# Kernel tuning notes

Hardware: AMD Instinct MI355X
Metric: run time of the kernel (lower is better)

The kernel has to match this reference:

```python
import jax, jax.numpy as jnp
import numpy as np

H = 128          # rnn_hid_size
SEQ_LEN = 2048
B = 4096
IN = 2           # SELECT_SIZE * 2


def _uniform(key, shape, stdv):
    return jax.random.uniform(key, shape, jnp.float32, -stdv, stdv)


def setup_inputs() -> dict:
    key = jax.random.key(0)
    ks = jax.random.split(key, 20)
    values = jax.random.normal(ks[0], (B, SEQ_LEN, 3), jnp.float32)
    masks = (jax.random.uniform(ks[1], (B, SEQ_LEN)) > 0.5).astype(jnp.float32)
    deltas = jax.random.uniform(ks[2], (B, SEQ_LEN, 3), jnp.float32)
    eval_masks = (jax.random.uniform(ks[3], (B, SEQ_LEN)) > 0.5).astype(jnp.float32)
    s = 1.0 / np.sqrt(H)
    params = {
        'Wih0': _uniform(ks[4], (4 * H, IN), s), 'Whh0': _uniform(ks[5], (4 * H, H), s),
        'bih0': _uniform(ks[6], (4 * H,), s), 'bhh0': _uniform(ks[7], (4 * H,), s),
        'Wih1': _uniform(ks[8], (4 * H, IN), s), 'Whh1': _uniform(ks[9], (4 * H, H), s),
        'bih1': _uniform(ks[10], (4 * H,), s), 'bhh1': _uniform(ks[11], (4 * H,), s),
        'td_W': _uniform(ks[12], (H, 1), s), 'td_b': _uniform(ks[13], (H,), s),
        'hr_W': _uniform(ks[14], (1, H), 1.0 / np.sqrt(H)), 'hr_b': _uniform(ks[15], (1,), 1.0 / np.sqrt(H)),
    }
    return dict(values=values, masks=masks, deltas=deltas, eval_masks=eval_masks, **params)


def _lstm_cell(x, h, c, Wih, Whh, bih, bhh):
    g = x @ Wih.T + bih + h @ Whh.T + bhh            # [B, 4H]
    i, f, gg, o = jnp.split(g, 4, axis=1)
    c2 = jax.nn.sigmoid(f) * c + jax.nn.sigmoid(i) * jnp.tanh(gg)
    h2 = jax.nn.sigmoid(o) * jnp.tanh(c2)
    return h2, c2


def reference(values, masks, deltas, eval_masks,
              Wih0, Whh0, bih0, bhh0, Wih1, Whh1, bih1, bhh1,
              td_W, td_b, hr_W, hr_b):
    bsize = values.shape[0]
    # time-major sequences for scan
    x_seq = jnp.transpose(values[:, :, 2:3], (1, 0, 2))      # [T, B, 1]
    m_seq = jnp.transpose(masks[:, :, None], (1, 0, 2))      # [T, B, 1]
    d_seq = jnp.transpose(deltas[:, :, 2:3], (1, 0, 2))      # [T, B, 1]
    in1_seq = jnp.transpose(values[:, :, 0:2], (1, 0, 2))    # [T, B, 2]

    h0 = jnp.zeros((bsize, H), jnp.float32)
    h1 = jnp.zeros((bsize, H), jnp.float32)
    c1 = jnp.zeros((bsize, H), jnp.float32)
    loss0 = jnp.zeros((), jnp.float32)

    def step(carry, inp):
        h0, h1, c1, loss = carry
        x_y, m_y, d_y, in1 = inp
        gamma_h = jnp.exp(-jax.nn.relu(d_y @ td_W.T + td_b))  # [B, H]
        x_h = h0 @ hr_W.T + hr_b                              # [B, 1]
        x_c = m_y * x_y + (1.0 - m_y) * x_h
        loss = loss + jnp.sum(jnp.square(x_y - x_h) * m_y) / (jnp.sum(m_y) + 1e-05)
        h1n, c1n = _lstm_cell(in1, h1, c1, Wih1, Whh1, bih1, bhh1)
        h1n = h1n * gamma_h
        inputs = jnp.concatenate([x_c, m_y], axis=1)          # [B, 2]
        h0n, _ = _lstm_cell(inputs, h1n, c1n, Wih0, Whh0, bih0, bhh0)
        return (h0n, h1n, c1n, loss), x_c

    (_, _, _, loss), imp = jax.lax.scan(step, (h0, h1, c1, loss0),
                                        (x_seq, m_seq, d_seq, in1_seq))
    imputations = jnp.transpose(imp, (1, 0, 2))               # [B, T, 1]
    evals = values[:, :, 2:3]
    return (loss, imputations, eval_masks[:, :, None], evals, masks[:, :, None])
```

## Files before the change

### kernel.cpp

```cpp
#include <hip/hip_runtime.h>

typedef __attribute__((ext_vector_type(8))) short bf16x8;
typedef __attribute__((ext_vector_type(4))) float f32x4;

#define L2E 1.4426950408889634f

__device__ __forceinline__ short f2bf(float x){
  unsigned u = __builtin_bit_cast(unsigned, x);
  u += 0x7fffu + ((u >> 16) & 1u);
  return (short)(u >> 16);
}
__device__ __forceinline__ float sigm(float x){
  float e = __builtin_amdgcn_exp2f(-x * L2E);
  return __builtin_amdgcn_rcpf(1.0f + e);
}
__device__ __forceinline__ float tanh_(float x){
  float e = __builtin_amdgcn_exp2f(x * (2.0f * L2E));
  return 1.0f - 2.0f * __builtin_amdgcn_rcpf(1.0f + e);
}

__global__ __launch_bounds__(512, 2)
void rios_main(const float* __restrict__ values, const float* __restrict__ masks,
               const float* __restrict__ deltas,
               const float* __restrict__ Wih0, const float* __restrict__ Whh0,
               const float* __restrict__ bih0, const float* __restrict__ bhh0,
               const float* __restrict__ Wih1, const float* __restrict__ Whh1,
               const float* __restrict__ bih1, const float* __restrict__ bhh1,
               const float* __restrict__ td_W, const float* __restrict__ td_b,
               const float* __restrict__ hr_W, const float* __restrict__ hr_b,
               float* __restrict__ out, float* __restrict__ lossws)
{
  __shared__ short hb[2][16][136];
  __shared__ float xh_part[8][16];
  __shared__ float xc_s[16];
  __shared__ float sA[2][5][16][16];

  const int tid = threadIdx.x;
  const int w  = tid >> 6;
  const int l  = tid & 63;
  const int q  = l >> 4;
  const int c  = l & 15;
  const int q4 = q << 2;
  const int u  = (w << 4) + c;
  const long long bb = (long long)blockIdx.x * 16;

  bf16x8 wf[2][4][4];
  {
    const float* WhhA[2] = { Whh1, Whh0 };
    #pragma unroll
    for (int cell = 0; cell < 2; ++cell)
      #pragma unroll
      for (int gi = 0; gi < 4; ++gi)
        #pragma unroll
        for (int kt = 0; kt < 4; ++kt){
          const float* rp = WhhA[cell] + (((gi << 7) + u) << 7) + (kt << 5) + (q << 3);
          bf16x8 f;
          #pragma unroll
          for (int j = 0; j < 8; ++j) f[j] = f2bf(rp[j]);
          wf[cell][gi][kt] = f;
        }
  }
  float wi[2][4][2], bs[2][4];
  {
    const float* WihA[2] = { Wih1, Wih0 };
    const float* bihA[2] = { bih1, bih0 };
    const float* bhhA[2] = { bhh1, bhh0 };
    #pragma unroll
    for (int cell = 0; cell < 2; ++cell)
      #pragma unroll
      for (int gi = 0; gi < 4; ++gi){
        int rg = (gi << 7) + u;
        wi[cell][gi][0] = WihA[cell][rg * 2];
        wi[cell][gi][1] = WihA[cell][rg * 2 + 1];
        bs[cell][gi]    = bihA[cell][rg] + bhhA[cell][rg];
      }
  }
  const float tdw = td_W[u], tdbv = td_b[u], hrw = hr_W[u], hrb = hr_b[0];

  {
    short* hz = &hb[0][0][0];
    for (int i = tid; i < 16 * 136; i += 512) hz[i] = 0;
    if (tid < 128) ((float*)xh_part)[tid] = 0.f;
  }

  const int isV = (tid < 192);
  const int isD = (tid >= 192 && tid < 384);
  const int isM = (tid >= 384 && tid < 448);
  int lb = 0, lp = 0;
  if (isV){ lb = tid / 12;        lp = tid % 12; }
  else if (isD){ lb = (tid-192)/12; lp = (tid-192)%12; }
  else if (isM){ lb = (tid-384)/4;  lp = (tid-384)%4; }
  const float* ldbase = nullptr;
  if (isV)      ldbase = values + ((bb + lb) * 2048LL) * 3 + lp * 4;
  else if (isD) ldbase = deltas + ((bb + lb) * 2048LL) * 3 + lp * 4;
  else if (isM) ldbase = masks  +  (bb + lb) * 2048LL      + lp * 4;

  auto write_stage = [&](int buf, f32x4 r){
    if (isV){
      #pragma unroll
      for (int j = 0; j < 4; ++j){ int idx = lp * 4 + j; sA[buf][idx % 3][idx / 3][lb] = r[j]; }
    } else if (isD){
      #pragma unroll
      for (int j = 0; j < 4; ++j){ int idx = lp * 4 + j; if (idx % 3 == 2) sA[buf][4][idx / 3][lb] = r[j]; }
    } else if (isM){
      #pragma unroll
      for (int j = 0; j < 4; ++j){ sA[buf][3][lp * 4 + j][lb] = r[j]; }
    }
  };

  if (tid < 448){
    f32x4 st = *(const f32x4*)(ldbase);
    write_stage(0, st);
  }
  __syncthreads();

  f32x4 c1 = {0.f, 0.f, 0.f, 0.f};

  for (int cc = 0; cc < 128; ++cc){
    const int cb = cc & 1;
    f32x4 nst;
    if (cc + 1 < 128 && tid < 448){
      long long t0 = (long long)(cc + 1) * 16;
      nst = *(const f32x4*)(ldbase + (isM ? t0 : t0 * 3));
    }
    #pragma unroll 2
    for (int tt = 0; tt < 16; ++tt){
      const int t = (cc << 4) + tt;
      const int p = tt & 1;

      f32x4 v0v = *(const f32x4*)&sA[cb][0][tt][q4];
      f32x4 v1v = *(const f32x4*)&sA[cb][1][tt][q4];
      f32x4 dv  = *(const f32x4*)&sA[cb][4][tt][q4];
      f32x4 acc[4];
      #pragma unroll
      for (int gi = 0; gi < 4; ++gi){
        #pragma unroll
        for (int r = 0; r < 4; ++r)
          acc[gi][r] = fmaf(v0v[r], wi[0][gi][0], fmaf(v1v[r], wi[0][gi][1], bs[0][gi]));
      }
      #pragma unroll
      for (int kt = 0; kt < 4; ++kt){
        bf16x8 af = *(const bf16x8*)&hb[p][c][(kt << 5) + (q << 3)];
        #pragma unroll
        for (int gi = 0; gi < 4; ++gi)
          acc[gi] = __builtin_amdgcn_mfma_f32_16x16x32_bf16(af, wf[0][gi][kt], acc[gi], 0, 0, 0);
      }

      if (w == 0){
        f32x4 xh = { hrb, hrb, hrb, hrb };
        #pragma unroll
        for (int w2 = 0; w2 < 8; ++w2)
          xh += *(const f32x4*)&xh_part[w2][q4];
        f32x4 xy = *(const f32x4*)&sA[cb][2][tt][q4];
        f32x4 mm = *(const f32x4*)&sA[cb][3][tt][q4];
        f32x4 xc = mm * xy + (1.f - mm) * xh;
        f32x4 df = xy - xh;
        f32x4 wv = df * df * mm;
        if (c == 0) *((f32x4*)&xc_s[q4]) = xc;
        float xcsel = (c == 0) ? xc[0] : ((c == 1) ? xc[1] : ((c == 2) ? xc[2] : xc[3]));
        if (c < 4) out[1 + (bb + q4 + c) * 2048LL + t] = xcsel;
        float swse = wv[0] + wv[1] + wv[2] + wv[3];
        float smm  = mm[0] + mm[1] + mm[2] + mm[3];
        swse += __shfl_xor(swse, 16); swse += __shfl_xor(swse, 32);
        smm  += __shfl_xor(smm, 16);  smm  += __shfl_xor(smm, 32);
        if (l == 0){ atomicAdd(&lossws[2 * t], swse); atomicAdd(&lossws[2 * t + 1], smm); }
      }

      #pragma unroll
      for (int r = 0; r < 4; ++r){
        float si = sigm(acc[0][r]);
        float sf = sigm(acc[1][r]);
        float tg = tanh_(acc[2][r]);
        float so = sigm(acc[3][r]);
        float c2 = sf * c1[r] + si * tg;
        float a1 = fmaxf(fmaf(dv[r], tdw, tdbv), 0.f);
        float gam = __builtin_amdgcn_exp2f(-a1 * L2E);
        float h1n = so * tanh_(c2) * gam;
        c1[r] = c2;
        hb[p ^ 1][q4 + r][u] = f2bf(h1n);
      }
      __syncthreads();

      f32x4 xcv = *(const f32x4*)&xc_s[q4];
      f32x4 mmv = *(const f32x4*)&sA[cb][3][tt][q4];
      #pragma unroll
      for (int gi = 0; gi < 4; ++gi){
        #pragma unroll
        for (int r = 0; r < 4; ++r)
          acc[gi][r] = fmaf(xcv[r], wi[1][gi][0], fmaf(mmv[r], wi[1][gi][1], bs[1][gi]));
      }
      #pragma unroll
      for (int kt = 0; kt < 4; ++kt){
        bf16x8 af = *(const bf16x8*)&hb[p ^ 1][c][(kt << 5) + (q << 3)];
        #pragma unroll
        for (int gi = 0; gi < 4; ++gi)
          acc[gi] = __builtin_amdgcn_mfma_f32_16x16x32_bf16(af, wf[1][gi][kt], acc[gi], 0, 0, 0);
      }
      f32x4 pv;
      #pragma unroll
      for (int r = 0; r < 4; ++r){
        float si = sigm(acc[0][r]);
        float sf = sigm(acc[1][r]);
        float tg = tanh_(acc[2][r]);
        float so = sigm(acc[3][r]);
        float c0n = sf * c1[r] + si * tg;
        float h0n = so * tanh_(c0n);
        pv[r] = h0n * hrw;
      }
      #pragma unroll
      for (int mk = 1; mk < 16; mk <<= 1){
        #pragma unroll
        for (int r = 0; r < 4; ++r) pv[r] += __shfl_xor(pv[r], mk);
      }
      if (c == 0) *((f32x4*)&xh_part[w][q4]) = pv;
      __syncthreads();
    }
    if (cc + 1 < 128 && tid < 448) write_stage(cb ^ 1, nst);
    __syncthreads();
  }
}

__global__ void loss_reduce(const float* __restrict__ lossws, float* __restrict__ out){
  __shared__ float red[1024];
  int t = threadIdx.x;
  float v = lossws[2 * t] / (lossws[2 * t + 1] + 1e-5f)
          + lossws[2 * (t + 1024)] / (lossws[2 * (t + 1024) + 1] + 1e-5f);
  red[t] = v;
  __syncthreads();
  for (int s = 512; s > 0; s >>= 1){
    if (t < s) red[t] += red[t + s];
    __syncthreads();
  }
  if (t == 0) out[0] = red[0];
}

__global__ void copy_outs(const float* __restrict__ values, const float* __restrict__ masks,
                          const float* __restrict__ evalm, float* __restrict__ out){
  const long long M = 8388608LL;
  long long i = (long long)blockIdx.x * 256 + threadIdx.x;
  if (i < M){
    out[1 + M     + i] = evalm[i];
    out[1 + 2 * M + i] = values[3 * i + 2];
    out[1 + 3 * M + i] = masks[i];
  }
}

extern "C" void kernel_launch(void* const* d_in, const int* in_sizes, int n_in,
                              void* d_out, int out_size, void* d_ws, size_t ws_size,
                              hipStream_t stream){
  const float* values = (const float*)d_in[0];
  const float* masks  = (const float*)d_in[1];
  const float* deltas = (const float*)d_in[2];
  const float* evalm  = (const float*)d_in[3];
  const float* Wih0   = (const float*)d_in[4];
  const float* Whh0   = (const float*)d_in[5];
  const float* bih0   = (const float*)d_in[6];
  const float* bhh0   = (const float*)d_in[7];
  const float* Wih1   = (const float*)d_in[8];
  const float* Whh1   = (const float*)d_in[9];
  const float* bih1   = (const float*)d_in[10];
  const float* bhh1   = (const float*)d_in[11];
  const float* td_W   = (const float*)d_in[12];
  const float* td_b   = (const float*)d_in[13];
  const float* hr_W   = (const float*)d_in[14];
  const float* hr_b   = (const float*)d_in[15];
  float* out    = (float*)d_out;
  float* lossws = (float*)d_ws;

  hipMemsetAsync(lossws, 0, 2048 * 2 * sizeof(float), stream);
  hipLaunchKernelGGL(copy_outs, dim3(32768), dim3(256), 0, stream, values, masks, evalm, out);
  hipLaunchKernelGGL(rios_main, dim3(256), dim3(512), 0, stream,
                     values, masks, deltas, Wih0, Whh0, bih0, bhh0,
                     Wih1, Whh1, bih1, bhh1, td_W, td_b, hr_W, hr_b, out, lossws);
  hipLaunchKernelGGL(loss_reduce, dim3(1), dim3(1024), 0, stream, lossws, out);
}
```

Measured before the change: 8.360 ms.

## Skew cell-0 by one step to fuse both LSTM cells under one barrier

Reorders the recurrence so that cell 0 for step s-1 and cell 1 for step s share one pass. Both read the same h1 buffer, so their MFMAs are interleaved and one __syncthreads per timestep is removed. x_c and the loss partials are now kept in shared memory, with imputation stores written out in batches of 16 and loss atomics done once per chunk rather than every step. A final epilogue drains the last step. This adds skewed-index bookkeeping, with some risk at the boundaries (s=0, chunk wrap, final step).

```diff
diff --git a/kernel.cpp b/kernel.cpp
--- a/kernel.cpp
+++ b/kernel.cpp
@@ -31,9 +31,10 @@
                float* __restrict__ out, float* __restrict__ lossws)
 {
   __shared__ short hb[2][16][136];
-  __shared__ float xh_part[8][16];
-  __shared__ float xc_s[16];
+  __shared__ float xh_part[2][8][16];
   __shared__ float sA[2][5][16][16];
+  __shared__ float loss_s[16][2];
+  __shared__ float xc_hist[16][16];
 
   const int tid = threadIdx.x;
   const int w  = tid >> 6;
@@ -80,7 +81,7 @@
   {
     short* hz = &hb[0][0][0];
     for (int i = tid; i < 16 * 136; i += 512) hz[i] = 0;
-    if (tid < 128) ((float*)xh_part)[tid] = 0.f;
+    if (tid < 256) ((float*)xh_part)[tid] = 0.f;
   }
 
   const int isV = (tid < 192);
@@ -125,98 +126,126 @@
     }
     #pragma unroll 2
     for (int tt = 0; tt < 16; ++tt){
-      const int t = (cc << 4) + tt;
+      const int s = (cc << 4) + tt;
       const int p = tt & 1;
+      const int o   = (s > 0) ? (s - 1) : 0;
+      const int ob  = (o >> 4) & 1;
+      const int ott = o & 15;
+
+      if (w == 0 && tt == 0 && cc > 0){
+        const int obase = s - 16;
+        const int m = l >> 2, j = l & 3;
+        #pragma unroll
+        for (int k = 0; k < 4; ++k)
+          out[1 + (bb + m) * 2048LL + obase + j * 4 + k] = xc_hist[j * 4 + k][m];
+        if (l < 32)
+          atomicAdd(&lossws[((obase + (l >> 1)) << 1) + (l & 1)], loss_s[l >> 1][l & 1]);
+      }
+
+      f32x4 xh = { hrb, hrb, hrb, hrb };
+      #pragma unroll
+      for (int w2 = 0; w2 < 8; ++w2)
+        xh += *(const f32x4*)&xh_part[p][w2][q4];
 
       f32x4 v0v = *(const f32x4*)&sA[cb][0][tt][q4];
       f32x4 v1v = *(const f32x4*)&sA[cb][1][tt][q4];
       f32x4 dv  = *(const f32x4*)&sA[cb][4][tt][q4];
-      f32x4 acc[4];
+      f32x4 xy  = *(const f32x4*)&sA[ob][2][ott][q4];
+      f32x4 mm  = *(const f32x4*)&sA[ob][3][ott][q4];
+      f32x4 xcv = mm * xy + (1.f - mm) * xh;
+
+      f32x4 acc1[4], acc0[4];
       #pragma unroll
       for (int gi = 0; gi < 4; ++gi){
         #pragma unroll
-        for (int r = 0; r < 4; ++r)
-          acc[gi][r] = fmaf(v0v[r], wi[0][gi][0], fmaf(v1v[r], wi[0][gi][1], bs[0][gi]));
+        for (int r = 0; r < 4; ++r){
+          acc1[gi][r] = fmaf(v0v[r], wi[0][gi][0], fmaf(v1v[r], wi[0][gi][1], bs[0][gi]));
+          acc0[gi][r] = fmaf(xcv[r], wi[1][gi][0], fmaf(mm[r],  wi[1][gi][1], bs[1][gi]));
+        }
       }
       #pragma unroll
       for (int kt = 0; kt < 4; ++kt){
         bf16x8 af = *(const bf16x8*)&hb[p][c][(kt << 5) + (q << 3)];
         #pragma unroll
-        for (int gi = 0; gi < 4; ++gi)
-          acc[gi] = __builtin_amdgcn_mfma_f32_16x16x32_bf16(af, wf[0][gi][kt], acc[gi], 0, 0, 0);
-      }
+        for (int gi = 0; gi < 4; ++gi){
+          acc1[gi] = __builtin_amdgcn_mfma_f32_16x16x32_bf16(af, wf[0][gi][kt], acc1[gi], 0, 0, 0);
+          acc0[gi] = __builtin_amdgcn_mfma_f32_16x16x32_bf16(af, wf[1][gi][kt], acc0[gi], 0, 0, 0);
+        }
+      }
+
+      f32x4 c_old = c1;
+      #pragma unroll
+      for (int r = 0; r < 4; ++r){
+        float si = sigm(acc1[0][r]);
+        float sf = sigm(acc1[1][r]);
+        float tg = tanh_(acc1[2][r]);
+        float so = sigm(acc1[3][r]);
+        float c2 = sf * c1[r] + si * tg;
+        float a1 = fmaxf(fmaf(dv[r], tdw, tdbv), 0.f);
+        float gam = __builtin_amdgcn_exp2f(-a1 * L2E);
+        c1[r] = c2;
+        hb[p ^ 1][q4 + r][u] = f2bf(so * tanh_(c2) * gam);
+      }
+
+      f32x4 pv;
+      #pragma unroll
+      for (int r = 0; r < 4; ++r){
+        float si = sigm(acc0[0][r]);
+        float sf = sigm(acc0[1][r]);
+        float tg = tanh_(acc0[2][r]);
+        float so = sigm(acc0[3][r]);
+        float c0n = sf * c_old[r] + si * tg;
+        pv[r] = so * tanh_(c0n) * hrw;
+      }
+      #pragma unroll
+      for (int mk = 1; mk < 16; mk <<= 1){
+        #pragma unroll
+        for (int r = 0; r < 4; ++r) pv[r] += __shfl_xor(pv[r], mk);
+      }
+      if (c == 0 && s > 0) *((f32x4*)&xh_part[p ^ 1][w][q4]) = pv;
 
       if (w == 0){
-        f32x4 xh = { hrb, hrb, hrb, hrb };
-        #pragma unroll
-        for (int w2 = 0; w2 < 8; ++w2)
-          xh += *(const f32x4*)&xh_part[w2][q4];
-        f32x4 xy = *(const f32x4*)&sA[cb][2][tt][q4];
-        f32x4 mm = *(const f32x4*)&sA[cb][3][tt][q4];
-        f32x4 xc = mm * xy + (1.f - mm) * xh;
         f32x4 df = xy - xh;
         f32x4 wv = df * df * mm;
-        if (c == 0) *((f32x4*)&xc_s[q4]) = xc;
-        float xcsel = (c == 0) ? xc[0] : ((c == 1) ? xc[1] : ((c == 2) ? xc[2] : xc[3]));
-        if (c < 4) out[1 + (bb + q4 + c) * 2048LL + t] = xcsel;
         float swse = wv[0] + wv[1] + wv[2] + wv[3];
         float smm  = mm[0] + mm[1] + mm[2] + mm[3];
         swse += __shfl_xor(swse, 16); swse += __shfl_xor(swse, 32);
         smm  += __shfl_xor(smm, 16);  smm  += __shfl_xor(smm, 32);
-        if (l == 0){ atomicAdd(&lossws[2 * t], swse); atomicAdd(&lossws[2 * t + 1], smm); }
-      }
-
-      #pragma unroll
-      for (int r = 0; r < 4; ++r){
-        float si = sigm(acc[0][r]);
-        float sf = sigm(acc[1][r]);
-        float tg = tanh_(acc[2][r]);
-        float so = sigm(acc[3][r]);
-        float c2 = sf * c1[r] + si * tg;
-        float a1 = fmaxf(fmaf(dv[r], tdw, tdbv), 0.f);
-        float gam = __builtin_amdgcn_exp2f(-a1 * L2E);
-        float h1n = so * tanh_(c2) * gam;
-        c1[r] = c2;
-        hb[p ^ 1][q4 + r][u] = f2bf(h1n);
-      }
-      __syncthreads();
-
-      f32x4 xcv = *(const f32x4*)&xc_s[q4];
-      f32x4 mmv = *(const f32x4*)&sA[cb][3][tt][q4];
-      #pragma unroll
-      for (int gi = 0; gi < 4; ++gi){
-        #pragma unroll
-        for (int r = 0; r < 4; ++r)
-          acc[gi][r] = fmaf(xcv[r], wi[1][gi][0], fmaf(mmv[r], wi[1][gi][1], bs[1][gi]));
-      }
-      #pragma unroll
-      for (int kt = 0; kt < 4; ++kt){
-        bf16x8 af = *(const bf16x8*)&hb[p ^ 1][c][(kt << 5) + (q << 3)];
-        #pragma unroll
-        for (int gi = 0; gi < 4; ++gi)
-          acc[gi] = __builtin_amdgcn_mfma_f32_16x16x32_bf16(af, wf[1][gi][kt], acc[gi], 0, 0, 0);
-      }
-      f32x4 pv;
-      #pragma unroll
-      for (int r = 0; r < 4; ++r){
-        float si = sigm(acc[0][r]);
-        float sf = sigm(acc[1][r]);
-        float tg = tanh_(acc[2][r]);
-        float so = sigm(acc[3][r]);
-        float c0n = sf * c1[r] + si * tg;
-        float h0n = so * tanh_(c0n);
-        pv[r] = h0n * hrw;
-      }
-      #pragma unroll
-      for (int mk = 1; mk < 16; mk <<= 1){
-        #pragma unroll
-        for (int r = 0; r < 4; ++r) pv[r] += __shfl_xor(pv[r], mk);
-      }
-      if (c == 0) *((f32x4*)&xh_part[w][q4]) = pv;
+        if (c == 0) *((f32x4*)&xc_hist[ott][q4]) = xcv;
+        if (l == 0){ loss_s[ott][0] = swse; loss_s[ott][1] = smm; }
+      }
+
+      if (tt == 15 && cc + 1 < 128 && tid < 448) write_stage(cb ^ 1, nst);
       __syncthreads();
     }
-    if (cc + 1 < 128 && tid < 448) write_stage(cb ^ 1, nst);
-    __syncthreads();
+  }
+
+  {
+    const int p = 0;
+    f32x4 xh = { hrb, hrb, hrb, hrb };
+    #pragma unroll
+    for (int w2 = 0; w2 < 8; ++w2)
+      xh += *(const f32x4*)&xh_part[p][w2][q4];
+    f32x4 xy = *(const f32x4*)&sA[1][2][15][q4];
+    f32x4 mm = *(const f32x4*)&sA[1][3][15][q4];
+    f32x4 xcv = mm * xy + (1.f - mm) * xh;
+    if (w == 0){
+      f32x4 df = xy - xh;
+      f32x4 wv = df * df * mm;
+      float swse = wv[0] + wv[1] + wv[2] + wv[3];
+      float smm  = mm[0] + mm[1] + mm[2] + mm[3];
+      swse += __shfl_xor(swse, 16); swse += __shfl_xor(swse, 32);
+      smm  += __shfl_xor(smm, 16);  smm  += __shfl_xor(smm, 32);
+      if (c == 0) *((f32x4*)&xc_hist[15][q4]) = xcv;
+      if (l == 0){ loss_s[15][0] = swse; loss_s[15][1] = smm; }
+      const int obase = 2032;
+      const int m = l >> 2, j = l & 3;
+      #pragma unroll
+      for (int k = 0; k < 4; ++k)
+        out[1 + (bb + m) * 2048LL + obase + j * 4 + k] = xc_hist[j * 4 + k][m];
+      if (l < 32)
+        atomicAdd(&lossws[((obase + (l >> 1)) << 1) + (l & 1)], loss_s[l >> 1][l & 1]);
+    }
   }
 }
 
```

Result: slower. 14.72 ms (+76.1%).

## Batch imputation stores and loss atomics per chunk; use LDS-only barriers

Applied to the files above, without the earlier changes.

Wave 0 used to write scattered per-timestep global stores and issue two global atomics every step, which sat on the serial recurrence path. It now stages the imputed values and per-step loss partials in shared-memory history buffers. Wave 7 flushes them once per 16-step chunk as vectorized stores and one batched atomic. The __syncthreads calls are replaced by a barrier that waits only on LDS counters, so outstanding global stores no longer stall every step. This adds shared memory and a little extra work for wave 7 at chunk boundaries.

```diff
diff --git a/kernel.cpp b/kernel.cpp
--- a/kernel.cpp
+++ b/kernel.cpp
@@ -17,6 +17,12 @@
 __device__ __forceinline__ float tanh_(float x){
   float e = __builtin_amdgcn_exp2f(x * (2.0f * L2E));
   return 1.0f - 2.0f * __builtin_amdgcn_rcpf(1.0f + e);
+}
+
+__device__ __forceinline__ void wg_barrier(){
+  asm volatile("s_waitcnt lgkmcnt(0)" ::: "memory");
+  __builtin_amdgcn_s_barrier();
+  asm volatile("" ::: "memory");
 }
 
 __global__ __launch_bounds__(512, 2)
@@ -32,8 +38,9 @@
 {
   __shared__ short hb[2][16][136];
   __shared__ float xh_part[8][16];
-  __shared__ float xc_s[16];
   __shared__ float sA[2][5][16][16];
+  __shared__ float xc_hist[2][16][16];
+  __shared__ float loss_s[2][16][2];
 
   const int tid = threadIdx.x;
   const int w  = tid >> 6;
@@ -125,8 +132,18 @@
     }
     #pragma unroll 2
     for (int tt = 0; tt < 16; ++tt){
-      const int t = (cc << 4) + tt;
       const int p = tt & 1;
+
+      if (w == 7 && tt == 0 && cc > 0){
+        const int obase = (cc - 1) << 4;
+        const int pb = cb ^ 1;
+        const int m = l >> 2, j = l & 3;
+        f32x4 st;
+        #pragma unroll
+        for (int k = 0; k < 4; ++k) st[k] = xc_hist[pb][(j << 2) + k][m];
+        *((f32x4*)&out[1 + (bb + m) * 2048LL + obase + (j << 2)]) = st;
+        if (l < 32) atomicAdd(&lossws[(obase << 1) + l], ((const float*)&loss_s[pb][0][0])[l]);
+      }
 
       f32x4 v0v = *(const f32x4*)&sA[cb][0][tt][q4];
       f32x4 v1v = *(const f32x4*)&sA[cb][1][tt][q4];
@@ -156,14 +173,12 @@
         f32x4 xc = mm * xy + (1.f - mm) * xh;
         f32x4 df = xy - xh;
         f32x4 wv = df * df * mm;
-        if (c == 0) *((f32x4*)&xc_s[q4]) = xc;
-        float xcsel = (c == 0) ? xc[0] : ((c == 1) ? xc[1] : ((c == 2) ? xc[2] : xc[3]));
-        if (c < 4) out[1 + (bb + q4 + c) * 2048LL + t] = xcsel;
+        if (c == 0) *((f32x4*)&xc_hist[cb][tt][q4]) = xc;
         float swse = wv[0] + wv[1] + wv[2] + wv[3];
         float smm  = mm[0] + mm[1] + mm[2] + mm[3];
         swse += __shfl_xor(swse, 16); swse += __shfl_xor(swse, 32);
         smm  += __shfl_xor(smm, 16);  smm  += __shfl_xor(smm, 32);
-        if (l == 0){ atomicAdd(&lossws[2 * t], swse); atomicAdd(&lossws[2 * t + 1], smm); }
+        if (l == 0){ loss_s[cb][tt][0] = swse; loss_s[cb][tt][1] = smm; }
       }
 
       #pragma unroll
@@ -179,9 +194,9 @@
         c1[r] = c2;
         hb[p ^ 1][q4 + r][u] = f2bf(h1n);
       }
-      __syncthreads();
-
-      f32x4 xcv = *(const f32x4*)&xc_s[q4];
+      wg_barrier();
+
+      f32x4 xcv = *(const f32x4*)&xc_hist[cb][tt][q4];
       f32x4 mmv = *(const f32x4*)&sA[cb][3][tt][q4];
       #pragma unroll
       for (int gi = 0; gi < 4; ++gi){
@@ -213,10 +228,20 @@
         for (int r = 0; r < 4; ++r) pv[r] += __shfl_xor(pv[r], mk);
       }
       if (c == 0) *((f32x4*)&xh_part[w][q4]) = pv;
-      __syncthreads();
+      wg_barrier();
     }
     if (cc + 1 < 128 && tid < 448) write_stage(cb ^ 1, nst);
-    __syncthreads();
+    wg_barrier();
+  }
+
+  if (w == 7){
+    const int obase = 2032;
+    const int m = l >> 2, j = l & 3;
+    f32x4 st;
+    #pragma unroll
+    for (int k = 0; k < 4; ++k) st[k] = xc_hist[1][(j << 2) + k][m];
+    *((f32x4*)&out[1 + (bb + m) * 2048LL + obase + (j << 2)]) = st;
+    if (l < 32) atomicAdd(&lossws[(obase << 1) + l], ((const float*)&loss_s[1][0][0])[l]);
   }
 }
 
```

Result: slower. 8.662 ms (+3.6%).
